# Kernel optimization log

Hardware: AMD Instinct MI355X
Metric: run time of the kernel (lower is better)

## Reference

```python
import jax, jax.numpy as jnp
import numpy as np
import math

SIZE = 64
SCALE = math.sqrt(SIZE)
EPS = 1e-12  # torch F.normalize default eps

def l2_normalize(x, axis):
    n = jnp.linalg.norm(x, ord=2, axis=axis, keepdims=True)
    return x / jnp.maximum(n, EPS)

def setup_inputs() -> dict:
    key = jax.random.key(0)
    k1, k2, k3 = jax.random.split(key, 3)
    n, l, s, d, v = 8, 2048, 2048, SIZE, SIZE
    return {
        "query": jax.random.normal(k1, (n, l, d), dtype=jnp.float32),
        "key": jax.random.normal(k2, (n, s, d), dtype=jnp.float32),
        "value": jax.random.normal(k3, (n, s, v), dtype=jnp.float32),
        "mask": jnp.ones((n, l, s), dtype=bool),
    }

def reference(query, key, value, mask):
    # rank-3 query path with normalize=True (cosine attention)
    q = l2_normalize(query, 2)
    k = l2_normalize(key, 2)
    score = jnp.einsum('nlk,nsk->nls', q, k) / SCALE
    score = jnp.where(mask, score, -jnp.inf)
    score = jax.nn.softmax(score, axis=2)  # [n, l, s]
    # equivalent to (score.unsqueeze(3) * value.unsqueeze(1)).sum(2)
    output_value = jnp.einsum('nls,nsv->nlv', score, value)
    return (output_value, score)
```

## Files before the change

kernel.cpp:

```cpp
#include <hip/hip_runtime.h>
#include <hip/hip_bf16.h>
#include <math.h>


typedef __bf16 bf16x8 __attribute__((ext_vector_type(8)));
typedef __bf16 bf16x4 __attribute__((ext_vector_type(4)));
typedef float f32x4 __attribute__((ext_vector_type(4)));

#define NB 8
#define LL 2048
#define SS 2048
#define DD 64
#define WORDS (SS / 32)
#define STRIP 512

__global__ __launch_bounds__(256) void pack_mask(const int* __restrict__ mask,
                                                 unsigned long long* __restrict__ bm) {
  const int w = threadIdx.x >> 6, lane = threadIdx.x & 63;
  const size_t gw = (size_t)blockIdx.x * 4 + w;
  const size_t stride = (size_t)gridDim.x * 4;
#pragma unroll
  for (int i = 0; i < 4; ++i) {
    size_t seg = gw + (size_t)i * stride;
    int m = __builtin_nontemporal_load(mask + seg * 64 + lane);
    unsigned long long b = __ballot(m != 0);
    if (lane == 0) bm[seg] = b;
  }
}

__global__ __launch_bounds__(256) void prep_norm(const float* __restrict__ q,
                                                 const float* __restrict__ k,
                                                 __bf16* __restrict__ Qb,
                                                 __bf16* __restrict__ Kb) {
  int w = threadIdx.x >> 6, lane = threadIdx.x & 63;
  int r = blockIdx.x * 4 + w;
  const float* src;
  __bf16* dst;
  float extra;
  if (r < NB * LL) {
    src = q + (size_t)r * DD;
    dst = Qb + (size_t)r * DD;
    extra = 0.125f;
  } else {
    int rk = r - NB * LL;
    src = k + (size_t)rk * DD;
    dst = Kb + (size_t)rk * DD;
    extra = 1.0f;
  }
  float x = src[lane];
  float ss = x * x;
  ss += __shfl_xor(ss, 1);
  ss += __shfl_xor(ss, 2);
  ss += __shfl_xor(ss, 4);
  ss += __shfl_xor(ss, 8);
  ss += __shfl_xor(ss, 16);
  ss += __shfl_xor(ss, 32);
  float nrm = sqrtf(ss);
  float sc = extra / fmaxf(nrm, 1e-12f);
  dst[lane] = (__bf16)(x * sc);
}

__global__ __launch_bounds__(256) void prep_vt(const float* __restrict__ v,
                                               __bf16* __restrict__ Vt) {
  __shared__ __bf16 tile[64][72];
  int n = blockIdx.y;
  int s0 = blockIdx.x * 64;
  int t = threadIdx.x;
#pragma unroll
  for (int it = 0; it < 4; ++it) {
    int idx = t + it * 256;
    int s = idx >> 4, c = idx & 15;
    float4 f = *(const float4*)(v + ((size_t)(n * SS + s0 + s)) * DD + c * 4);
    tile[s][c * 4 + 0] = (__bf16)f.x;
    tile[s][c * 4 + 1] = (__bf16)f.y;
    tile[s][c * 4 + 2] = (__bf16)f.z;
    tile[s][c * 4 + 3] = (__bf16)f.w;
  }
  __syncthreads();
#pragma unroll
  for (int it = 0; it < 4; ++it) {
    int idx = t + it * 256;
    int vv = idx >> 4, c = idx & 15;
    bf16x4 o;
    o[0] = tile[c * 4 + 0][vv];
    o[1] = tile[c * 4 + 1][vv];
    o[2] = tile[c * 4 + 2][vv];
    o[3] = tile[c * 4 + 3][vv];
    *(bf16x4*)(Vt + ((size_t)(n * DD + vv)) * SS + s0 + c * 4) = o;
  }
}

__global__ __launch_bounds__(256, 4) void attn_main(const __bf16* __restrict__ Qb,
                                                    const __bf16* __restrict__ Kb,
                                                    const __bf16* __restrict__ Vt,
                                                    const unsigned* __restrict__ bm32,
                                                    float* __restrict__ out_val,
                                                    float* __restrict__ out_score) {
  __shared__ char smem[22784];
  __bf16(*e_lds)[2][16][72] = (__bf16(*)[2][16][72])smem;
  unsigned(*bm_t)[16] = (unsigned(*)[16])(smem + 18432);
  float(*rs_lds)[16] = (float(*)[16])(smem + 22528);
  float(*o_lds)[16][64] = (float(*)[16][64])smem;

  const int n = blockIdx.y;
  const int l0 = blockIdx.x * 16;
  const int t = threadIdx.x;
  const int w = t >> 6;
  const int lane = t & 63;
  const int m16 = lane & 15;
  const int quad = lane >> 4;

  {
    int word = t & 63, wv = t >> 6;
#pragma unroll
    for (int i = 0; i < 4; ++i) {
      int row = wv * 4 + i;
      bm_t[word][row] = bm32[(((size_t)(n * LL + l0 + row)) << 6) + word];
    }
  }

  const __bf16* qrow = Qb + ((size_t)(n * LL + l0 + m16)) * DD;
  bf16x8 aq0 = *(const bf16x8*)(qrow + quad * 8);
  bf16x8 aq1 = *(const bf16x8*)(qrow + 32 + quad * 8);

  const __bf16* kbase = Kb + (size_t)n * SS * DD;
  const __bf16* vbase = Vt + (size_t)n * DD * SS;
  const size_t mrow_base = ((size_t)(n * LL + l0)) * SS;
  const int sbase = w * STRIP;

  f32x4 acc_o[4] = {{0.f, 0.f, 0.f, 0.f}, {0.f, 0.f, 0.f, 0.f},
                    {0.f, 0.f, 0.f, 0.f}, {0.f, 0.f, 0.f, 0.f}};
  float rsum[4] = {0.f, 0.f, 0.f, 0.f};

  __syncthreads();

  for (int c = 0; c < STRIP / 64; ++c) {
    const int s0 = sbase + c * 64;
    f32x4 acc[4];
#pragma unroll
    for (int ct = 0; ct < 4; ++ct) {
      const __bf16* krow = kbase + (size_t)(s0 + ct * 16 + m16) * DD;
      bf16x8 kb0 = *(const bf16x8*)(krow + quad * 8);
      bf16x8 kb1 = *(const bf16x8*)(krow + 32 + quad * 8);
      f32x4 a = {0.f, 0.f, 0.f, 0.f};
      a = __builtin_amdgcn_mfma_f32_16x16x32_bf16(aq0, kb0, a, 0, 0, 0);
      a = __builtin_amdgcn_mfma_f32_16x16x32_bf16(aq1, kb1, a, 0, 0, 0);
      acc[ct] = a;
    }
    const int bw = s0 >> 5;
    const uint4 mw0 = *(const uint4*)&bm_t[bw][quad * 4];
    const uint4 mw1 = *(const uint4*)&bm_t[bw + 1][quad * 4];
#pragma unroll
    for (int ct = 0; ct < 4; ++ct) {
      const unsigned sh = (unsigned)((ct * 16 + m16) & 31);
#pragma unroll
      for (int r = 0; r < 4; ++r) {
        unsigned wd = (ct < 2) ? (&mw0.x)[r] : (&mw1.x)[r];
        unsigned mk = (wd >> sh) & 1u;
        float e = mk ? __expf(acc[ct][r]) : 0.0f;
        rsum[r] += e;
        e_lds[w][c & 1][quad * 4 + r][ct * 16 + m16] = (__bf16)e;
      }
    }
    bf16x8 ae0 = *(const bf16x8*)(&e_lds[w][c & 1][m16][quad * 8]);
    bf16x8 ae1 = *(const bf16x8*)(&e_lds[w][c & 1][m16][32 + quad * 8]);
#pragma unroll
    for (int vt = 0; vt < 4; ++vt) {
      const __bf16* vrow = vbase + (size_t)(vt * 16 + m16) * SS + s0;
      bf16x8 vb0 = *(const bf16x8*)(vrow + quad * 8);
      bf16x8 vb1 = *(const bf16x8*)(vrow + 32 + quad * 8);
      acc_o[vt] = __builtin_amdgcn_mfma_f32_16x16x32_bf16(ae0, vb0, acc_o[vt], 0, 0, 0);
      acc_o[vt] = __builtin_amdgcn_mfma_f32_16x16x32_bf16(ae1, vb1, acc_o[vt], 0, 0, 0);
    }
  }

#pragma unroll
  for (int r = 0; r < 4; ++r) {
    float s = rsum[r];
    s += __shfl_xor(s, 1);
    s += __shfl_xor(s, 2);
    s += __shfl_xor(s, 4);
    s += __shfl_xor(s, 8);
    rsum[r] = s;
  }

  __syncthreads();

#pragma unroll
  for (int vt = 0; vt < 4; ++vt)
#pragma unroll
    for (int r = 0; r < 4; ++r) o_lds[w][quad * 4 + r][vt * 16 + m16] = acc_o[vt][r];
  if (m16 == 0) {
#pragma unroll
    for (int r = 0; r < 4; ++r) rs_lds[w][quad * 4 + r] = rsum[r];
  }
  __syncthreads();

  float inv[4];
#pragma unroll
  for (int r = 0; r < 4; ++r) {
    int row = quad * 4 + r;
    float s = rs_lds[0][row] + rs_lds[1][row] + rs_lds[2][row] + rs_lds[3][row];
    inv[r] = 1.0f / s;
  }
#pragma unroll
  for (int r = 0; r < 4; ++r) {
    int row = quad * 4 + r;
    float o = o_lds[0][row][16 * w + m16] + o_lds[1][row][16 * w + m16] +
              o_lds[2][row][16 * w + m16] + o_lds[3][row][16 * w + m16];
    out_val[((size_t)(n * LL + l0 + row)) * DD + 16 * w + m16] = o * inv[r];
  }

  for (int c = 0; c < STRIP / 64; ++c) {
    const int s0 = sbase + c * 64;
    f32x4 acc[4];
#pragma unroll
    for (int ct = 0; ct < 4; ++ct) {
      const __bf16* krow = kbase + (size_t)(s0 + ct * 16 + m16) * DD;
      bf16x8 kb0 = *(const bf16x8*)(krow + quad * 8);
      bf16x8 kb1 = *(const bf16x8*)(krow + 32 + quad * 8);
      f32x4 a = {0.f, 0.f, 0.f, 0.f};
      a = __builtin_amdgcn_mfma_f32_16x16x32_bf16(aq0, kb0, a, 0, 0, 0);
      a = __builtin_amdgcn_mfma_f32_16x16x32_bf16(aq1, kb1, a, 0, 0, 0);
      acc[ct] = a;
    }
    const int bw = s0 >> 5;
    const uint4 mw0 = *(const uint4*)&bm_t[bw][quad * 4];
    const uint4 mw1 = *(const uint4*)&bm_t[bw + 1][quad * 4];
#pragma unroll
    for (int ct = 0; ct < 4; ++ct) {
      const unsigned sh = (unsigned)((ct * 16 + m16) & 31);
#pragma unroll
      for (int r = 0; r < 4; ++r) {
        unsigned wd = (ct < 2) ? (&mw0.x)[r] : (&mw1.x)[r];
        unsigned mk = (wd >> sh) & 1u;
        float val = mk ? __expf(acc[ct][r]) * inv[r] : 0.0f;
        out_score[mrow_base + (size_t)(quad * 4 + r) * SS + s0 + ct * 16 + m16] = val;
      }
    }
  }
}

extern "C" void kernel_launch(void* const* d_in, const int* in_sizes, int n_in,
                              void* d_out, int out_size, void* d_ws, size_t ws_size,
                              hipStream_t stream) {
  const float* q = (const float*)d_in[0];
  const float* k = (const float*)d_in[1];
  const float* v = (const float*)d_in[2];
  const int* mask = (const int*)d_in[3];

  float* out_val = (float*)d_out;
  float* out_score = out_val + (size_t)NB * LL * DD;

  __bf16* Qb = (__bf16*)d_ws;
  __bf16* Kb = Qb + (size_t)NB * LL * DD;
  __bf16* Vt = Kb + (size_t)NB * SS * DD;
  unsigned long long* bm = (unsigned long long*)(Vt + (size_t)NB * DD * SS);

  pack_mask<<<dim3(32768), dim3(256), 0, stream>>>(mask, bm);
  prep_norm<<<dim3((NB * LL * 2) / 4), dim3(256), 0, stream>>>(q, k, Qb, Kb);
  prep_vt<<<dim3(SS / 64, NB), dim3(256), 0, stream>>>(v, Vt);
  attn_main<<<dim3(LL / 16, NB), dim3(256), 0, stream>>>(Qb, Kb, Vt, (const unsigned*)bm,
                                                         out_val, out_score);
}
```

Measured before the change: 340.7 us.

## Fuse mask bit-packing into attention kernel and split keys across eight waves

Drops the separate pack_mask kernel and packs the boolean mask into LDS bitmasks inside attn_main using ballots on the raw int mask rows. The block grows to 512 threads (8 waves), each covering a 256-key strip, and the final cross-wave reduction of output and row sums is rewritten for 8 slots. It removes one launch and the round trip of the packed mask through global memory. In exchange each block must read the full int mask for its 16 rows before starting, which serialises that load ahead of compute, and LDS use per block nearly doubles.

```diff
diff --git a/kernel.cpp b/kernel.cpp
--- a/kernel.cpp
+++ b/kernel.cpp
@@ -11,22 +11,7 @@
 #define LL 2048
 #define SS 2048
 #define DD 64
-#define WORDS (SS / 32)
-#define STRIP 512
-
-__global__ __launch_bounds__(256) void pack_mask(const int* __restrict__ mask,
-                                                 unsigned long long* __restrict__ bm) {
-  const int w = threadIdx.x >> 6, lane = threadIdx.x & 63;
-  const size_t gw = (size_t)blockIdx.x * 4 + w;
-  const size_t stride = (size_t)gridDim.x * 4;
-#pragma unroll
-  for (int i = 0; i < 4; ++i) {
-    size_t seg = gw + (size_t)i * stride;
-    int m = __builtin_nontemporal_load(mask + seg * 64 + lane);
-    unsigned long long b = __ballot(m != 0);
-    if (lane == 0) bm[seg] = b;
-  }
-}
+#define STRIP 256
 
 __global__ __launch_bounds__(256) void prep_norm(const float* __restrict__ q,
                                                  const float* __restrict__ k,
@@ -90,17 +75,17 @@
   }
 }
 
-__global__ __launch_bounds__(256, 4) void attn_main(const __bf16* __restrict__ Qb,
+__global__ __launch_bounds__(512, 8) void attn_main(const __bf16* __restrict__ Qb,
                                                     const __bf16* __restrict__ Kb,
                                                     const __bf16* __restrict__ Vt,
-                                                    const unsigned* __restrict__ bm32,
+                                                    const int* __restrict__ mask,
                                                     float* __restrict__ out_val,
                                                     float* __restrict__ out_score) {
-  __shared__ char smem[22784];
+  __shared__ char smem[40960];
   __bf16(*e_lds)[2][16][72] = (__bf16(*)[2][16][72])smem;
-  unsigned(*bm_t)[16] = (unsigned(*)[16])(smem + 18432);
-  float(*rs_lds)[16] = (float(*)[16])(smem + 22528);
-  float(*o_lds)[16][64] = (float(*)[16][64])smem;
+  unsigned(*bm_t)[16] = (unsigned(*)[16])(smem + 36864);
+  float(*o_slot)[16][64] = (float(*)[16][64])smem;
+  float(*rs_lds)[16] = (float(*)[16])(smem + 32768);
 
   const int n = blockIdx.y;
   const int l0 = blockIdx.x * 16;
@@ -111,11 +96,23 @@
   const int quad = lane >> 4;
 
   {
-    int word = t & 63, wv = t >> 6;
-#pragma unroll
-    for (int i = 0; i < 4; ++i) {
-      int row = wv * 4 + i;
-      bm_t[word][row] = bm32[(((size_t)(n * LL + l0 + row)) << 6) + word];
+#pragma unroll
+    for (int rr = 0; rr < 2; ++rr) {
+      const int row = 2 * w + rr;
+      const int* mrow = mask + (size_t)(n * LL + l0 + row) * SS;
+      for (int sb = 0; sb < 32; sb += 8) {
+        int mv[8];
+#pragma unroll
+        for (int j = 0; j < 8; ++j) mv[j] = mrow[(sb + j) * 64 + lane];
+#pragma unroll
+        for (int j = 0; j < 8; ++j) {
+          unsigned long long b = __ballot(mv[j] != 0);
+          if (lane == 0) {
+            bm_t[2 * (sb + j)][row] = (unsigned)b;
+            bm_t[2 * (sb + j) + 1][row] = (unsigned)(b >> 32);
+          }
+        }
+      }
     }
   }
 
@@ -136,7 +133,9 @@
 
   for (int c = 0; c < STRIP / 64; ++c) {
     const int s0 = sbase + c * 64;
-    f32x4 acc[4];
+    const int bw = s0 >> 5;
+    const uint4 mw0 = *(const uint4*)&bm_t[bw][quad * 4];
+    const uint4 mw1 = *(const uint4*)&bm_t[bw + 1][quad * 4];
 #pragma unroll
     for (int ct = 0; ct < 4; ++ct) {
       const __bf16* krow = kbase + (size_t)(s0 + ct * 16 + m16) * DD;
@@ -145,19 +144,11 @@
       f32x4 a = {0.f, 0.f, 0.f, 0.f};
       a = __builtin_amdgcn_mfma_f32_16x16x32_bf16(aq0, kb0, a, 0, 0, 0);
       a = __builtin_amdgcn_mfma_f32_16x16x32_bf16(aq1, kb1, a, 0, 0, 0);
-      acc[ct] = a;
-    }
-    const int bw = s0 >> 5;
-    const uint4 mw0 = *(const uint4*)&bm_t[bw][quad * 4];
-    const uint4 mw1 = *(const uint4*)&bm_t[bw + 1][quad * 4];
-#pragma unroll
-    for (int ct = 0; ct < 4; ++ct) {
       const unsigned sh = (unsigned)((ct * 16 + m16) & 31);
 #pragma unroll
       for (int r = 0; r < 4; ++r) {
         unsigned wd = (ct < 2) ? (&mw0.x)[r] : (&mw1.x)[r];
-        unsigned mk = (wd >> sh) & 1u;
-        float e = mk ? __expf(acc[ct][r]) : 0.0f;
+        float e = ((wd >> sh) & 1u) ? __expf(a[r]) : 0.0f;
         rsum[r] += e;
         e_lds[w][c & 1][quad * 4 + r][ct * 16 + m16] = (__bf16)e;
       }
@@ -189,31 +180,41 @@
 #pragma unroll
   for (int vt = 0; vt < 4; ++vt)
 #pragma unroll
-    for (int r = 0; r < 4; ++r) o_lds[w][quad * 4 + r][vt * 16 + m16] = acc_o[vt][r];
+    for (int r = 0; r < 4; ++r) o_slot[w][quad * 4 + r][vt * 16 + m16] = acc_o[vt][r];
   if (m16 == 0) {
 #pragma unroll
     for (int r = 0; r < 4; ++r) rs_lds[w][quad * 4 + r] = rsum[r];
   }
   __syncthreads();
+
+#pragma unroll
+  for (int e = 0; e < 2; ++e) {
+    int el = t + e * 512;
+    int row = el >> 6, col = el & 63;
+    float o = 0.f, s = 0.f;
+#pragma unroll
+    for (int j = 0; j < 8; ++j) {
+      o += o_slot[j][row][col];
+      s += rs_lds[j][row];
+    }
+    out_val[((size_t)(n * LL + l0 + row)) * DD + col] = o / s;
+  }
 
   float inv[4];
 #pragma unroll
   for (int r = 0; r < 4; ++r) {
     int row = quad * 4 + r;
-    float s = rs_lds[0][row] + rs_lds[1][row] + rs_lds[2][row] + rs_lds[3][row];
+    float s = 0.f;
+#pragma unroll
+    for (int j = 0; j < 8; ++j) s += rs_lds[j][row];
     inv[r] = 1.0f / s;
-  }
-#pragma unroll
-  for (int r = 0; r < 4; ++r) {
-    int row = quad * 4 + r;
-    float o = o_lds[0][row][16 * w + m16] + o_lds[1][row][16 * w + m16] +
-              o_lds[2][row][16 * w + m16] + o_lds[3][row][16 * w + m16];
-    out_val[((size_t)(n * LL + l0 + row)) * DD + 16 * w + m16] = o * inv[r];
   }
 
   for (int c = 0; c < STRIP / 64; ++c) {
     const int s0 = sbase + c * 64;
-    f32x4 acc[4];
+    const int bw = s0 >> 5;
+    const uint4 mw0 = *(const uint4*)&bm_t[bw][quad * 4];
+    const uint4 mw1 = *(const uint4*)&bm_t[bw + 1][quad * 4];
 #pragma unroll
     for (int ct = 0; ct < 4; ++ct) {
       const __bf16* krow = kbase + (size_t)(s0 + ct * 16 + m16) * DD;
@@ -222,19 +223,11 @@
       f32x4 a = {0.f, 0.f, 0.f, 0.f};
       a = __builtin_amdgcn_mfma_f32_16x16x32_bf16(aq0, kb0, a, 0, 0, 0);
       a = __builtin_amdgcn_mfma_f32_16x16x32_bf16(aq1, kb1, a, 0, 0, 0);
-      acc[ct] = a;
-    }
-    const int bw = s0 >> 5;
-    const uint4 mw0 = *(const uint4*)&bm_t[bw][quad * 4];
-    const uint4 mw1 = *(const uint4*)&bm_t[bw + 1][quad * 4];
-#pragma unroll
-    for (int ct = 0; ct < 4; ++ct) {
       const unsigned sh = (unsigned)((ct * 16 + m16) & 31);
 #pragma unroll
       for (int r = 0; r < 4; ++r) {
         unsigned wd = (ct < 2) ? (&mw0.x)[r] : (&mw1.x)[r];
-        unsigned mk = (wd >> sh) & 1u;
-        float val = mk ? __expf(acc[ct][r]) * inv[r] : 0.0f;
+        float val = ((wd >> sh) & 1u) ? __expf(a[r]) * inv[r] : 0.0f;
         out_score[mrow_base + (size_t)(quad * 4 + r) * SS + s0 + ct * 16 + m16] = val;
       }
     }
@@ -255,11 +248,9 @@
   __bf16* Qb = (__bf16*)d_ws;
   __bf16* Kb = Qb + (size_t)NB * LL * DD;
   __bf16* Vt = Kb + (size_t)NB * SS * DD;
-  unsigned long long* bm = (unsigned long long*)(Vt + (size_t)NB * DD * SS);
-
-  pack_mask<<<dim3(32768), dim3(256), 0, stream>>>(mask, bm);
+
   prep_norm<<<dim3((NB * LL * 2) / 4), dim3(256), 0, stream>>>(q, k, Qb, Kb);
   prep_vt<<<dim3(SS / 64, NB), dim3(256), 0, stream>>>(v, Vt);
-  attn_main<<<dim3(LL / 16, NB), dim3(256), 0, stream>>>(Qb, Kb, Vt, (const unsigned*)bm,
+  attn_main<<<dim3(LL / 16, NB), dim3(512), 0, stream>>>(Qb, Kb, Vt, mask,
                                                          out_val, out_score);
 }
```

Result: slower. 448.1 us (+31.5%).
